# Performance work log

Hardware: AMD Instinct MI355X
Metric: run time of the kernel (lower is better)

## Reference

```python
import jax, jax.numpy as jnp
import numpy as np
from jax import lax

EPS = 1e-5
MIN_SAMPLES = 4
RESHAPE = 14        # edge-map downsample factor
KEEP_FRAC = 0.1     # 1 - quantile(0.9)
KERNEL_FRAC = 0.05  # eval-mode log_kernel

SOBEL_X = jnp.array([[-1., 0., 1.], [-2., 0., 2.], [-1., 0., 1.]], jnp.float32)
SOBEL_Y = jnp.array([[-1., -2., -1.], [0., 0., 0.], [1., 2., 1.]], jnp.float32)


def _dwconv3(x, k):
    C = x.shape[1]
    kern = jnp.broadcast_to(k, (C, 1, 3, 3)).astype(x.dtype)
    return lax.conv_general_dilated(x, kern, (1, 1), 'SAME',
        feature_group_count=C, dimension_numbers=('NCHW', 'OIHW', 'NCHW'))


def _erode3(m):
    k = jnp.ones((1, 1, 3, 3), m.dtype)
    s = lax.conv_general_dilated(m, k, (1, 1), 'SAME',
        dimension_numbers=('NCHW', 'OIHW', 'NCHW'))
    return (s >= 9.0).astype(m.dtype)


def _masked_mean(x, mask, axis=-1):
    m = mask.astype(x.dtype)
    return jnp.sum(x * m, axis=axis) / jnp.maximum(jnp.sum(m, axis=axis), 1.0)


def _ssi_norm(x, mask):
    # scale-shift-invariant normalization: masked median shift, masked MAD scale
    big = jnp.where(mask, x, jnp.inf)
    srt = jnp.sort(big, axis=-1)
    n = jnp.sum(mask, axis=-1)
    idx = jnp.maximum((n - 1) // 2, 0)
    med = jnp.take_along_axis(srt, idx[..., None], axis=-1)
    med = jnp.where(n[..., None] > 0, med, 0.0)
    scale = _masked_mean(jnp.abs(x - med), mask, axis=-1)[..., None]
    return (x - med) / jnp.maximum(scale, EPS)


def _get_edge(image, vmask):
    gx = _dwconv3(image, SOBEL_X) / 8.0
    gy = _dwconv3(image, SOBEL_Y) / 8.0
    gx = jnp.sqrt(jnp.mean(gx * gx, axis=1, keepdims=True))
    gy = jnp.sqrt(jnp.mean(gy * gy, axis=1, keepdims=True))
    edges = jnp.sqrt(gx * gx + gy * gy)
    H, W = edges.shape[-2:]
    bm = jnp.zeros((H, W), edges.dtype).at[3:H - 3, 3:W - 3].set(1.0)
    return edges * bm * vmask


def _resize_bilinear(x, oh, ow):
    # torch F.interpolate bilinear, align_corners=False, no antialias
    B, C, H, W = x.shape
    def coords(o, s):
        c = jnp.clip((jnp.arange(o) + 0.5) * (s / o) - 0.5, 0.0, s - 1.0)
        i0 = jnp.floor(c).astype(jnp.int32)
        return i0, jnp.minimum(i0 + 1, s - 1), c - i0
    y0, y1, wy = coords(oh, H)
    x0, x1, wx = coords(ow, W)
    wy = wy[:, None]; wx = wx[None, :]
    g = lambda yi, xi: x[:, :, yi[:, None], xi[None, :]]
    return (g(y0, x0) * (1 - wy) * (1 - wx) + g(y0, x1) * (1 - wy) * wx
          + g(y1, x0) * wy * (1 - wx) + g(y1, x1) * wy * wx)


def _sample_edges(edges):
    B, _, H, W = edges.shape
    oh, ow = H // RESHAPE, W // RESHAPE
    e = _resize_bilinear(edges, oh, ow).reshape(B, -1)
    k = max(int(KEEP_FRAC * oh * ow), 10)
    _, idx = lax.top_k(e, k)
    return jnp.stack([(idx // ow) * RESHAPE, (idx % ow) * RESHAPE], -1).astype(jnp.int32)


def _extract_patches(x, coords, kh, kw):
    # vectorized irregular patch gather: [B,C,H,W] + [B,P,2] -> [B,P*C,kh*kw]
    B, C, H, W = x.shape
    ph, pw = kh // 2, kw // 2
    xp = jnp.pad(x, ((0, 0), (0, 0), (ph, ph), (pw, pw)))
    dy = jnp.arange(-ph, ph + 1)
    dx = jnp.arange(-pw, pw + 1)
    def one(img, y, x_):
        return img[:, (y + dy)[:, None], (x_ + dx)[None, :]]
    patches = jax.vmap(jax.vmap(one, in_axes=(None, 0, 0)))(
        xp, coords[..., 0] + ph, coords[..., 1] + pw)  # [B,P,C,kh,kw]
    return patches.reshape(B, -1, kh * kw)


def _forward(inp, tgt, mask, image, vmask):
    mask = mask.astype(bool)
    inp = inp.astype(jnp.float32)
    tgt = tgt.astype(jnp.float32)
    B, _, H, W = inp.shape
    vm = _erode3(vmask.astype(jnp.float32))
    edges = _get_edge(image.astype(jnp.float32), vm)
    coords = _sample_edges(edges)
    ks = int(KERNEL_FRAC * min(H, W))
    ks += int(ks % 2 == 0)
    # local patch branch
    pin = _extract_patches(inp, coords, ks, ks)
    ptg = _extract_patches(tgt, coords, ks, ks)
    pmk = _extract_patches(mask.astype(jnp.float32), coords, ks, ks) > 0.5
    pin = _ssi_norm(pin, pmk)
    ptg = _ssi_norm(ptg, pmk)
    err = jnp.maximum(jnp.abs(pin - ptg), EPS)
    valid = jnp.sum(pmk, axis=-1) >= MIN_SAMPLES
    ep = jnp.sqrt(jnp.maximum(_masked_mean(err, pmk, -1), EPS))  # [B,P]
    e_patch = _masked_mean(ep, valid, -1)                         # [B]
    # global image branch
    gi = _ssi_norm(inp.reshape(B, 1, H * W), mask.reshape(B, 1, H * W))
    gt = _ssi_norm(tgt.reshape(B, 1, H * W), mask.reshape(B, 1, H * W))
    gerr = jnp.maximum(jnp.abs(gi - gt), EPS)
    e_glob = jnp.sqrt(jnp.maximum(_masked_mean(gerr, mask.reshape(B, 1, H * W), -1), EPS)).squeeze(-1)
    return 0.5 * (e_patch + e_glob)  # [B]


def setup_inputs() -> dict:
    key = jax.random.key(0)
    k1, k2, k3, k4 = jax.random.split(key, 4)
    B, H, W = 32, 480, 640
    return {
        'input': jax.random.uniform(k1, (B, 1, H, W), jnp.float32, 0.1, 10.0),
        'target': jax.random.uniform(k2, (B, 1, H, W), jnp.float32, 0.1, 10.0),
        'mask': jax.random.bernoulli(k3, 0.9, (B, 1, H, W)),
        'image': jax.random.normal(k4, (B, 3, H, W), jnp.float32),
        'validity_mask': jnp.ones((B, 1, H, W), bool),
    }


def reference(input, target, mask, image, validity_mask):
    return _forward(input, target, mask, image, validity_mask)
```

## Files before the change

### kernel.cpp

```cpp
#include <hip/hip_runtime.h>
#include <math.h>

#define BB 32
#define HH 480
#define WW 640
#define HWN (HH * WW)
#define OH 34
#define OW 45
#define OHW (OH * OW)
#define KTOP 153
#define KS 25
#define PHW 12
#define PATCH (KS * KS)
#define RESHAPE_I 14
#define EPSV 1e-5f

#define TSLICE 10
#define TSW (OHW / TSLICE)

#define NB12 4096
#define PSLICE 32
#define NSLICE 16
#define CAP 32768
#define LCAP 2048
#define CPAD 32

__device__ __forceinline__ unsigned int fkey(float f) {
  unsigned int u = __float_as_uint(f);
  return (u & 0x80000000u) ? ~u : (u | 0x80000000u);
}
__device__ __forceinline__ float fkey_inv(unsigned int k) {
  unsigned int u = (k & 0x80000000u) ? (k & 0x7FFFFFFFu) : ~k;
  return __uint_as_float(u);
}

__device__ __forceinline__ float breduce256(float v, float* red) {
  const int t = threadIdx.x;
  __syncthreads();
  red[t] = v;
  __syncthreads();
  for (int s2 = 128; s2 > 0; s2 >>= 1) {
    if (t < s2) red[t] += red[t + s2];
    __syncthreads();
  }
  float r = red[0];
  __syncthreads();
  return r;
}

__device__ __forceinline__ float2 breduce256x2(float a, float b, float* red) {
  const int t = threadIdx.x;
  __syncthreads();
  red[t] = a;
  red[256 + t] = b;
  __syncthreads();
  for (int s2 = 128; s2 > 0; s2 >>= 1) {
    if (t < s2) {
      red[t] += red[t + s2];
      red[256 + t] += red[256 + t + s2];
    }
    __syncthreads();
  }
  float2 r = make_float2(red[0], red[256]);
  __syncthreads();
  return r;
}

__device__ float edge_at(const float* __restrict__ image, const unsigned char* __restrict__ vmask,
                         int b, int y, int x) {
  if (y < 3 || y >= HH - 3 || x < 3 || x >= WW - 3) return 0.f;
  const unsigned char* vm = vmask + (size_t)b * HWN;
  #pragma unroll
  for (int dy = -1; dy <= 1; ++dy) {
    #pragma unroll
    for (int dx = -1; dx <= 1; ++dx) {
      if (!vm[(size_t)(y + dy) * WW + (x + dx)]) return 0.f;
    }
  }
  const float* img = image + (size_t)b * 3 * HWN;
  float sx2 = 0.f, sy2 = 0.f;
  #pragma unroll
  for (int c = 0; c < 3; ++c) {
    const float* p = img + (size_t)c * HWN + (size_t)y * WW + x;
    float a00 = p[-WW - 1], a01 = p[-WW], a02 = p[-WW + 1];
    float a10 = p[-1],                    a12 = p[1];
    float a20 = p[WW - 1],  a21 = p[WW],  a22 = p[WW + 1];
    float gx = (-a00 + a02 + -2.f * a10 + 2.f * a12 + -a20 + a22) / 8.f;
    float gy = (-a00 + -2.f * a01 + -a02 + a20 + 2.f * a21 + a22) / 8.f;
    sx2 += gx * gx;
    sy2 += gy * gy;
  }
  float gxm = sqrtf(sx2 / 3.f);
  float gym = sqrtf(sy2 / 3.f);
  return sqrtf(gxm * gxm + gym * gym);
}

__global__ __launch_bounds__(256) void edge_resize_kernel(const float* __restrict__ image,
                                                          const unsigned char* __restrict__ vmask,
                                                          float* __restrict__ re) {
  int gid = blockIdx.x * 256 + threadIdx.x;
  int corner = gid & 3;
  int cell = gid >> 2;
  int b = cell / OHW;
  int rem = cell % OHW;
  int oy = rem / OW, ox = rem % OW;

  const float ry = (float)((double)HH / (double)OH);
  const float rx = (float)((double)WW / (double)OW);
  float cy = fminf(fmaxf(((float)oy + 0.5f) * ry - 0.5f, 0.f), (float)(HH - 1));
  float cx = fminf(fmaxf(((float)ox + 0.5f) * rx - 0.5f, 0.f), (float)(WW - 1));
  int y0 = (int)floorf(cy);
  int x0 = (int)floorf(cx);
  int y1 = min(y0 + 1, HH - 1);
  int x1 = min(x0 + 1, WW - 1);
  float wy = cy - (float)y0;
  float wx = cx - (float)x0;

  int yy = (corner & 2) ? y1 : y0;
  int xx = (corner & 1) ? x1 : x0;
  float w = ((corner & 2) ? wy : 1.f - wy) * ((corner & 1) ? wx : 1.f - wx);
  float g = edge_at(image, vmask, b, yy, xx) * w;
  g += __shfl_xor(g, 1, 64);
  g += __shfl_xor(g, 2, 64);
  if (corner == 0) re[cell] = g;
}

__global__ __launch_bounds__(256) void topk_rank_kernel(const float* __restrict__ re,
                                                        int* __restrict__ rpart) {
  const int b = blockIdx.x / TSLICE;
  const int sl = blockIdx.x % TSLICE;
  const int t = threadIdx.x;
  __shared__ float e[OHW];
  for (int i = t; i < OHW; i += 256) e[i] = re[b * OHW + i];
  __syncthreads();

  float vi[6];
  int idx[6], cnt[6];
  #pragma unroll
  for (int q = 0; q < 6; ++q) {
    int i = t + q * 256;
    idx[q] = i;
    vi[q] = (i < OHW) ? e[i] : 0.f;
    cnt[q] = 0;
  }
  const int j0 = sl * TSW;
  for (int jj = 0; jj < TSW; ++jj) {
    int j = j0 + jj;
    float u = e[j];
    #pragma unroll
    for (int q = 0; q < 6; ++q) {
      cnt[q] += (u > vi[q]) || (u == vi[q] && j < idx[q]);
    }
  }
  int* rp = rpart + ((size_t)b * TSLICE + sl) * OHW;
  #pragma unroll
  for (int q = 0; q < 6; ++q) {
    if (idx[q] < OHW) rp[idx[q]] = cnt[q];
  }
}

__global__ __launch_bounds__(256) void topk_write_kernel(const int* __restrict__ rpart,
                                                         int* __restrict__ coords) {
  const int b = blockIdx.x;
  const int t = threadIdx.x;
  const int* rp = rpart + (size_t)b * TSLICE * OHW;
  for (int i = t; i < OHW; i += 256) {
    int rank = 0;
    #pragma unroll
    for (int sl = 0; sl < TSLICE; ++sl) rank += rp[sl * OHW + i];
    if (rank < KTOP) {
      coords[(b * KTOP + rank) * 2 + 0] = (i / OW) * RESHAPE_I;
      coords[(b * KTOP + rank) * 2 + 1] = (i % OW) * RESHAPE_I;
    }
  }
}

__global__ __launch_bounds__(64, 4) void patch_kernel(const float* __restrict__ inp,
                                                      const float* __restrict__ tgt,
                                                      const unsigned char* __restrict__ mask,
                                                      const int* __restrict__ coords,
                                                      float* __restrict__ ep, float* __restrict__ val) {
  const int bk = blockIdx.x;
  const int b = bk / KTOP;
  const int t = threadIdx.x;
  __shared__ unsigned int hist[512];
  __shared__ unsigned int sh_pref[2];
  __shared__ int sh_rank[2];

  const int cy = coords[bk * 2 + 0];
  const int cx = coords[bk * 2 + 1];

  float v_in[10], v_tg[10];
  unsigned int mbits = 0;
  #pragma unroll
  for (int q = 0; q < 10; ++q) {
    int i = t + q * 64;
    float vi = 0.f, vt = 0.f;
    if (i < PATCH) {
      int dy = i / KS - PHW, dx = i % KS - PHW;
      int y = cy + dy, x = cx + dx;
      if (y >= 0 && y < HH && x >= 0 && x < WW) {
        size_t off = (size_t)b * HWN + (size_t)y * WW + x;
        if (mask[off]) mbits |= (1u << q);
        vi = inp[off];
        vt = tgt[off];
      }
    }
    v_in[q] = vi; v_tg[q] = vt;
  }

  int pn = __popc(mbits);
  #pragma unroll
  for (int d = 32; d > 0; d >>= 1) pn += __shfl_xor(pn, d, 64);
  const int n = pn;
  const float nf = (float)n;
  const int r = (n > 0) ? ((n - 1) >> 1) : 0;

  if (t == 0) {
    sh_pref[0] = 0; sh_pref[1] = 0;
    sh_rank[0] = r; sh_rank[1] = r;
  }
  __syncthreads();

  #pragma unroll
  for (int p = 0; p < 4; ++p) {
    const int shift = 24 - 8 * p;
    #pragma unroll
    for (int j = 0; j < 8; ++j) hist[t + 64 * j] = 0;
    __syncthreads();
    const int r_in = sh_rank[0], r_tg = sh_rank[1];
    const unsigned int pref_in = sh_pref[0], pref_tg = sh_pref[1];
    #pragma unroll
    for (int q = 0; q < 10; ++q) {
      if (mbits & (1u << q)) {
        unsigned int k = fkey(v_in[q]);
        if (p == 0 || (k >> (shift + 8)) == pref_in)
          atomicAdd(&hist[(k >> shift) & 255u], 1u);
        unsigned int k2 = fkey(v_tg[q]);
        if (p == 0 || (k2 >> (shift + 8)) == pref_tg)
          atomicAdd(&hist[256 + ((k2 >> shift) & 255u)], 1u);
      }
    }
    __syncthreads();
    {
      unsigned int a0 = hist[t * 4 + 0], a1 = hist[t * 4 + 1];
      unsigned int a2 = hist[t * 4 + 2], a3 = hist[t * 4 + 3];
      unsigned int b0 = hist[256 + t * 4 + 0], b1 = hist[256 + t * 4 + 1];
      unsigned int b2 = hist[256 + t * 4 + 2], b3 = hist[256 + t * 4 + 3];
      unsigned int sa0 = a0, sa1 = sa0 + a1, sa2 = sa1 + a2, sa3 = sa2 + a3;
      unsigned int sb0 = b0, sb1 = sb0 + b1, sb2 = sb1 + b2, sb3 = sb2 + b3;
      unsigned int ta = sa3, tb = sb3;
      #pragma unroll
      for (int d = 1; d < 64; d <<= 1) {
        unsigned int ua = (unsigned int)__shfl_up((int)ta, d, 64);
        unsigned int ub = (unsigned int)__shfl_up((int)tb, d, 64);
        if (t >= d) { ta += ua; tb += ub; }
      }
      unsigned int exa = ta - sa3, exb = tb - sb3;
      unsigned int rra = (unsigned int)r_in, rrb = (unsigned int)r_tg;
      unsigned int pa[4] = {exa, exa + sa0, exa + sa1, exa + sa2};
      unsigned int ca[4] = {exa + sa0, exa + sa1, exa + sa2, exa + sa3};
      unsigned int pb[4] = {exb, exb + sb0, exb + sb1, exb + sb2};
      unsigned int cb[4] = {exb + sb0, exb + sb1, exb + sb2, exb + sb3};
      #pragma unroll
      for (int j = 0; j < 4; ++j) {
        if (rra >= pa[j] && rra < ca[j]) {
          sh_pref[0] = (pref_in << 8) | (unsigned int)(t * 4 + j);
          sh_rank[0] = (int)(rra - pa[j]);
        }
        if (rrb >= pb[j] && rrb < cb[j]) {
          sh_pref[1] = (pref_tg << 8) | (unsigned int)(t * 4 + j);
          sh_rank[1] = (int)(rrb - pb[j]);
        }
      }
    }
    __syncthreads();
  }

  const float med_i = (n > 0) ? fkey_inv(sh_pref[0]) : 0.f;
  const float med_t = (n > 0) ? fkey_inv(sh_pref[1]) : 0.f;

  float pi = 0.f, pt = 0.f;
  #pragma unroll
  for (int q = 0; q < 10; ++q) {
    if (mbits & (1u << q)) {
      pi += fabsf(v_in[q] - med_i);
      pt += fabsf(v_tg[q] - med_t);
    }
  }
  #pragma unroll
  for (int d = 32; d > 0; d >>= 1) {
    pi += __shfl_xor(pi, d, 64);
    pt += __shfl_xor(pt, d, 64);
  }
  const float si = fmaxf(pi / fmaxf(nf, 1.f), EPSV);
  const float st = fmaxf(pt / fmaxf(nf, 1.f), EPSV);

  float pe = 0.f;
  #pragma unroll
  for (int q = 0; q < 10; ++q) {
    if (mbits & (1u << q)) {
      float a = (v_in[q] - med_i) / si;
      float c = (v_tg[q] - med_t) / st;
      pe += fmaxf(fabsf(a - c), EPSV);
    }
  }
  #pragma unroll
  for (int d = 32; d > 0; d >>= 1) pe += __shfl_xor(pe, d, 64);

  if (t == 0) {
    ep[bk] = sqrtf(fmaxf(pe / fmaxf(nf, 1.f), EPSV));
    val[bk] = (n >= 4) ? 1.f : 0.f;
  }
}

__global__ __launch_bounds__(256) void preduce_kernel(const float* __restrict__ ep,
                                                      const float* __restrict__ val,
                                                      float* __restrict__ e_patch) {
  const int b = blockIdx.x;
  const int t = threadIdx.x;
  __shared__ float red[512];
  float se = 0.f, sv = 0.f;
  for (int i = t; i < KTOP; i += 256) {
    float v = val[b * KTOP + i];
    se += ep[b * KTOP + i] * v;
    sv += v;
  }
  float2 tt = breduce256x2(se, sv, red);
  if (t == 0) e_patch[b] = tt.x / fmaxf(tt.y, 1.f);
}

__global__ __launch_bounds__(256) void gpass12_kernel(const float* __restrict__ inp,
                                                      const float* __restrict__ tgt,
                                                      const unsigned char* __restrict__ mask,
                                                      unsigned int* __restrict__ ghist) {
  const int b = blockIdx.x / PSLICE;
  const int sl = blockIdx.x % PSLICE;
  const int t = threadIdx.x;
  __shared__ unsigned int hist[2 * NB12];
  for (int i = t; i < 2 * NB12; i += 256) hist[i] = 0;
  __syncthreads();
  const float4* xi4 = (const float4*)(inp + (size_t)b * HWN);
  const float4* xt4 = (const float4*)(tgt + (size_t)b * HWN);
  const unsigned int* m4 = (const unsigned int*)(mask + (size_t)b * HWN);
  const int per4 = (HWN / PSLICE) / 4;
  const int s0 = sl * per4;
  for (int i = s0 + t; i < s0 + per4; i += 256) {
    unsigned int mm = m4[i];
    if (!mm) continue;
    float4 a = xi4[i], c = xt4[i];
    if (mm & 0x000000FFu) { atomicAdd(&hist[fkey(a.x) >> 20], 1u); atomicAdd(&hist[NB12 + (fkey(c.x) >> 20)], 1u); }
    if (mm & 0x0000FF00u) { atomicAdd(&hist[fkey(a.y) >> 20], 1u); atomicAdd(&hist[NB12 + (fkey(c.y) >> 20)], 1u); }
    if (mm & 0x00FF0000u) { atomicAdd(&hist[fkey(a.z) >> 20], 1u); atomicAdd(&hist[NB12 + (fkey(c.z) >> 20)], 1u); }
    if (mm & 0xFF000000u) { atomicAdd(&hist[fkey(a.w) >> 20], 1u); atomicAdd(&hist[NB12 + (fkey(c.w) >> 20)], 1u); }
  }
  __syncthreads();
  for (int i = t; i < NB12; i += 256) {
    unsigned int h0 = hist[i], h1 = hist[NB12 + i];
    if (h0) atomicAdd(&ghist[(size_t)(b * 2 + 0) * NB12 + i], h0);
    if (h1) atomicAdd(&ghist[(size_t)(b * 2 + 1) * NB12 + i], h1);
  }
}

__global__ __launch_bounds__(256) void gsel12_kernel(const unsigned int* __restrict__ ghist,
                                                     int* __restrict__ sel) {
  const int bs = blockIdx.x;
  const int t = threadIdx.x;
  const unsigned int* gh = ghist + (size_t)bs * NB12;
  __shared__ unsigned int scan[256];
  unsigned int local[16];
  unsigned int s = 0;
  const int base = t * 16;
  #pragma unroll
  for (int j = 0; j < 16; ++j) {
    local[j] = gh[base + j];
    s += local[j];
  }
  scan[t] = s;
  __syncthreads();
  for (int d = 1; d < 256; d <<= 1) {
    unsigned int v = (t >= d) ? scan[t - d] : 0u;
    __syncthreads();
    scan[t] += v;
    __syncthreads();
  }
  const unsigned int incl = scan[t];
  const unsigned int ex = incl - s;
  const unsigned int n = scan[255];
  if (n == 0) {
    if (t == 0) {
      sel[bs * 4 + 0] = -1;
      sel[bs * 4 + 1] = 0;
      sel[bs * 4 + 2] = 0;
      sel[bs * 4 + 3] = 0;
    }
    return;
  }
  const unsigned int r = (n - 1) >> 1;
  if (r >= ex && r < incl) {
    unsigned int cum = ex;
    int bin = base;
    #pragma unroll
    for (int j = 0; j < 16; ++j) {
      unsigned int h = local[j];
      if (cum + h > r) { bin = base + j; break; }
      cum += h;
    }
    sel[bs * 4 + 0] = bin;
    sel[bs * 4 + 1] = (int)(r - cum);
    sel[bs * 4 + 2] = (int)n;
    sel[bs * 4 + 3] = (int)cum;
  }
}

__global__ __launch_bounds__(256) void gcollect_kernel(const float* __restrict__ inp,
                                                       const float* __restrict__ tgt,
                                                       const unsigned char* __restrict__ mask,
                                                       const int* __restrict__ sel,
                                                       float* __restrict__ cand,
                                                       unsigned int* __restrict__ ccount,
                                                       float* __restrict__ sbelow,
                                                       float* __restrict__ sabove) {
  const int bs = blockIdx.x / NSLICE;
  const int sl = blockIdx.x % NSLICE;
  const int b = bs >> 1, s = bs & 1;
  const float* x = (s == 0 ? inp : tgt) + (size_t)b * HWN;
  const unsigned char* m = mask + (size_t)b * HWN;
  const int prefix = sel[bs * 4 + 0];
  __shared__ float red[512];
  __shared__ float buf[LCAP];
  __shared__ unsigned int lcnt, gbase;
  const int t = threadIdx.x;
  if (t == 0) lcnt = 0;
  __syncthreads();
  float sb = 0.f, sa = 0.f;
  if (prefix >= 0) {
    float* cd = cand + (size_t)bs * CAP;
    const float4* x4 = (const float4*)x;
    const unsigned int* m4 = (const unsigned int*)m;
    const int per4 = (HWN / NSLICE) / 4;
    const int s0 = sl * per4;
    for (int i = s0 + t; i < s0 + per4; i += 256) {
      unsigned int mm = m4[i];
      if (!mm) continue;
      float4 a = x4[i];
      #define GCOL(av, bit) \
        if (mm & bit) { \
          float v = av; \
          int pf = (int)(fkey(v) >> 20); \
          if (pf < prefix) sb += v; \
          else if (pf > prefix) sa += v; \
          else { \
            unsigned int pos = atomicAdd(&lcnt, 1u); \
            if (pos < LCAP) buf[pos] = v; \
            else { \
              unsigned int g = atomicAdd(&ccount[bs * CPAD], 1u); \
              if (g < CAP) cd[g] = v; \
            } \
          } \
        }
      GCOL(a.x, 0x000000FFu)
      GCOL(a.y, 0x0000FF00u)
      GCOL(a.z, 0x00FF0000u)
      GCOL(a.w, 0xFF000000u)
      #undef GCOL
    }
  }
  __syncthreads();
  if (prefix >= 0) {
    unsigned int c = min(lcnt, (unsigned int)LCAP);
    if (t == 0 && c > 0) gbase = atomicAdd(&ccount[bs * CPAD], c);
    __syncthreads();
    if (c > 0) {
      float* cd = cand + (size_t)bs * CAP;
      unsigned int base = gbase;
      for (unsigned int i = t; i < c; i += 256) {
        unsigned int pos = base + i;
        if (pos < CAP) cd[pos] = buf[i];
      }
    }
  }
  float2 ts = breduce256x2(sb, sa, red);
  if (t == 0) {
    atomicAdd(&sbelow[bs], ts.x);
    atomicAdd(&sabove[bs], ts.y);
  }
}

__global__ __launch_bounds__(256) void gfinal_kernel(const float* __restrict__ cand,
                                                     const unsigned int* __restrict__ ccount,
                                                     const int* __restrict__ sel,
                                                     const float* __restrict__ sbelow,
                                                     const float* __restrict__ sabove,
                                                     float* __restrict__ gstats,
                                                     float* __restrict__ nvals) {
  const int bs = blockIdx.x;
  const int t = threadIdx.x;
  const int prefix = sel[bs * 4 + 0];
  const int r2 = sel[bs * 4 + 1];
  const int n = sel[bs * 4 + 2];
  const int nbelow = sel[bs * 4 + 3];
  __shared__ unsigned int hist[256];
  __shared__ float red[256];
  __shared__ int sh_bin, sh_r;
  __shared__ float sh_med;
  const float* cd = cand + (size_t)bs * CAP;
  int c = (int)min(ccount[bs * CPAD], (unsigned int)CAP);
  if (prefix < 0) {
    if (t == 0) {
      gstats[bs * 2 + 0] = 0.f;
      gstats[bs * 2 + 1] = 0.f;
      if ((bs & 1) == 0) nvals[bs >> 1] = 0.f;
    }
    return;
  }

  hist[t] = 0;
  __syncthreads();
  for (int i = t; i < c; i += 256)
    atomicAdd(&hist[(fkey(cd[i]) >> 12) & 255u], 1u);
  __syncthreads();
  if (t == 0) {
    unsigned int rr = (unsigned int)r2, cum = 0;
    int bin = 0;
    for (; bin < 256; ++bin) {
      unsigned int h = hist[bin];
      if (cum + h > rr) break;
      cum += h;
    }
    sh_bin = bin;
    sh_r = (int)(rr - cum);
  }
  __syncthreads();
  const int bin1 = sh_bin;
  const int r3 = sh_r;

  hist[t] = 0;
  __syncthreads();
  for (int i = t; i < c; i += 256) {
    unsigned int k = fkey(cd[i]);
    if (((k >> 12) & 255u) == (unsigned int)bin1)
      atomicAdd(&hist[(k >> 4) & 255u], 1u);
  }
  __syncthreads();
  if (t == 0) {
    unsigned int rr = (unsigned int)r3, cum = 0;
    int bin = 0;
    for (; bin < 256; ++bin) {
      unsigned int h = hist[bin];
      if (cum + h > rr) break;
      cum += h;
    }
    sh_bin = bin;
    sh_r = (int)(rr - cum);
  }
  __syncthreads();
  const int bin2 = sh_bin;
  const int r4 = sh_r;

  if (t < 16) hist[t] = 0;
  __syncthreads();
  {
    const unsigned int want = (((unsigned int)bin1 << 8) | (unsigned int)bin2);
    for (int i = t; i < c; i += 256) {
      unsigned int k = fkey(cd[i]);
      if (((k >> 4) & 0xFFFFu) == want)
        atomicAdd(&hist[k & 15u], 1u);
    }
  }
  __syncthreads();
  if (t == 0) {
    unsigned int rr = (unsigned int)r4, cum = 0;
    int bin = 0;
    for (; bin < 16; ++bin) {
      unsigned int h = hist[bin];
      if (cum + h > rr) break;
      cum += h;
    }
    unsigned int key = ((unsigned int)prefix << 20) |
                       ((unsigned int)bin1 << 12) |
                       ((unsigned int)bin2 << 4) | (unsigned int)bin;
    sh_med = fkey_inv(key);
  }
  __syncthreads();
  const float med = sh_med;

  float ps = 0.f;
  for (int i = t; i < c; i += 256) ps += fabsf(cd[i] - med);
  float scand = breduce256(ps, red);
  if (t == 0) {
    float nb = (float)nbelow;
    float na = (float)(n - nbelow - c);
    float num = (nb * med - sbelow[bs]) + (sabove[bs] - na * med) + scand;
    gstats[bs * 2 + 0] = med;
    gstats[bs * 2 + 1] = num / fmaxf((float)n, 1.f);
    if ((bs & 1) == 0) nvals[bs >> 1] = (float)n;
  }
}

__global__ __launch_bounds__(256) void gerr_kernel(const float* __restrict__ inp,
                                                   const float* __restrict__ tgt,
                                                   const unsigned char* __restrict__ mask,
                                                   const float* __restrict__ gstats,
                                                   float* __restrict__ gacc) {
  const int b = blockIdx.x / PSLICE;
  const int sl = blockIdx.x % PSLICE;
  __shared__ float red[256];
  const int t = threadIdx.x;
  const float med_i = gstats[(b * 2 + 0) * 2 + 0];
  const float sc_i = fmaxf(gstats[(b * 2 + 0) * 2 + 1], EPSV);
  const float med_t = gstats[(b * 2 + 1) * 2 + 0];
  const float sc_t = fmaxf(gstats[(b * 2 + 1) * 2 + 1], EPSV);
  const float ri = 1.f / sc_i, rt = 1.f / sc_t;
  const float4* xi4 = (const float4*)(inp + (size_t)b * HWN);
  const float4* xt4 = (const float4*)(tgt + (size_t)b * HWN);
  const unsigned int* m4 = (const unsigned int*)(mask + (size_t)b * HWN);
  const int per4 = (HWN / PSLICE) / 4;
  const int s0 = sl * per4;
  float part = 0.f;
  for (int i = s0 + t; i < s0 + per4; i += 256) {
    unsigned int mm = m4[i];
    if (!mm) continue;
    float4 a = xi4[i], c = xt4[i];
    if (mm & 0x000000FFu) part += fmaxf(fabsf((a.x - med_i) * ri - (c.x - med_t) * rt), EPSV);
    if (mm & 0x0000FF00u) part += fmaxf(fabsf((a.y - med_i) * ri - (c.y - med_t) * rt), EPSV);
    if (mm & 0x00FF0000u) part += fmaxf(fabsf((a.z - med_i) * ri - (c.z - med_t) * rt), EPSV);
    if (mm & 0xFF000000u) part += fmaxf(fabsf((a.w - med_i) * ri - (c.w - med_t) * rt), EPSV);
  }
  float tp = breduce256(part, red);
  if (t == 0) atomicAdd(&gacc[b], tp);
}

__global__ __launch_bounds__(64) void final_kernel(const float* __restrict__ gacc,
                                                   const float* __restrict__ nvals,
                                                   const float* __restrict__ e_patch,
                                                   float* __restrict__ out) {
  const int b = threadIdx.x;
  if (b < BB) {
    float n = nvals[b];
    float eg = sqrtf(fmaxf(gacc[b] / fmaxf(n, 1.f), EPSV));
    out[b] = 0.5f * (e_patch[b] + eg);
  }
}

extern "C" void kernel_launch(void* const* d_in, const int* in_sizes, int n_in,
                              void* d_out, int out_size, void* d_ws, size_t ws_size,
                              hipStream_t stream) {
  const float* inp = (const float*)d_in[0];
  const float* tgt = (const float*)d_in[1];
  const unsigned char* mask = (const unsigned char*)d_in[2];
  const float* image = (const float*)d_in[3];
  const unsigned char* vmask = (const unsigned char*)d_in[4];
  float* out = (float*)d_out;

  float* ws = (float*)d_ws;
  float* re = ws;
  int* coords = (int*)(ws + 48960);
  float* ep = ws + 48960 + 9792;
  float* val = ep + 4896;
  float* e_patch = val + 4896;
  float* gstats = e_patch + 32;
  float* nvals = gstats + 128;
  int* sel12 = (int*)(nvals + 32);
  float* cand = (float*)(sel12 + 256);
  unsigned int* ghist12 = (unsigned int*)(cand + (size_t)64 * CAP);
  unsigned int* ccount = ghist12 + (size_t)64 * NB12;
  float* sbelow = (float*)(ccount + 64 * CPAD);
  float* sabove = sbelow + 64;
  float* gacc = sabove + 64;
  size_t zero_bytes = ((size_t)64 * NB12 + 64 * CPAD + 64 + 64 + 32) * 4;
  hipMemsetAsync(ghist12, 0, zero_bytes, stream);

  int* rpart = (int*)cand;

  edge_resize_kernel<<<(BB * OHW * 4) / 256, 256, 0, stream>>>(image, vmask, re);
  topk_rank_kernel<<<BB * TSLICE, 256, 0, stream>>>(re, rpart);
  topk_write_kernel<<<BB, 256, 0, stream>>>(rpart, coords);
  patch_kernel<<<BB * KTOP, 64, 0, stream>>>(inp, tgt, mask, coords, ep, val);
  preduce_kernel<<<BB, 256, 0, stream>>>(ep, val, e_patch);
  gpass12_kernel<<<BB * PSLICE, 256, 0, stream>>>(inp, tgt, mask, ghist12);
  gsel12_kernel<<<BB * 2, 256, 0, stream>>>(ghist12, sel12);
  gcollect_kernel<<<BB * 2 * NSLICE, 256, 0, stream>>>(inp, tgt, mask, sel12, cand, ccount, sbelow, sabove);
  gfinal_kernel<<<BB * 2, 256, 0, stream>>>(cand, ccount, sel12, sbelow, sabove, gstats, nvals);
  gerr_kernel<<<BB * PSLICE, 256, 0, stream>>>(inp, tgt, mask, gstats, gacc);
  final_kernel<<<1, 64, 0, stream>>>(gacc, nvals, e_patch, out);
}
```

Baseline: 393.2 us.

## Merge independent kernels into shared launches and fold the final reduction into gerr

```diff
diff --git a/kernel.cpp b/kernel.cpp
--- a/kernel.cpp
+++ b/kernel.cpp
@@ -25,6 +25,10 @@
 #define LCAP 2048
 #define CPAD 32
 
+#define EDGE_BLKS ((BB * OHW * 4) / 256)
+#define RANK_BLKS (BB * TSLICE)
+#define COL_BLKS (BB * 2 * NSLICE)
+
 __device__ __forceinline__ unsigned int fkey(float f) {
   unsigned int u = __float_as_uint(f);
   return (u & 0x80000000u) ? ~u : (u | 0x80000000u);
@@ -93,6 +97,38 @@
   float gxm = sqrtf(sx2 / 3.f);
   float gym = sqrtf(sy2 / 3.f);
   return sqrtf(gxm * gxm + gym * gym);
+}
+
+__global__ __launch_bounds__(256) void gpass12_kernel(const float* __restrict__ inp,
+                                                      const float* __restrict__ tgt,
+                                                      const unsigned char* __restrict__ mask,
+                                                      unsigned int* __restrict__ ghist) {
+  const int b = blockIdx.x / PSLICE;
+  const int sl = blockIdx.x % PSLICE;
+  const int t = threadIdx.x;
+  __shared__ unsigned int hist[2 * NB12];
+  for (int i = t; i < 2 * NB12; i += 256) hist[i] = 0;
+  __syncthreads();
+  const float4* xi4 = (const float4*)(inp + (size_t)b * HWN);
+  const float4* xt4 = (const float4*)(tgt + (size_t)b * HWN);
+  const unsigned int* m4 = (const unsigned int*)(mask + (size_t)b * HWN);
+  const int per4 = (HWN / PSLICE) / 4;
+  const int s0 = sl * per4;
+  for (int i = s0 + t; i < s0 + per4; i += 256) {
+    unsigned int mm = m4[i];
+    if (!mm) continue;
+    float4 a = xi4[i], c = xt4[i];
+    if (mm & 0x000000FFu) { atomicAdd(&hist[fkey(a.x) >> 20], 1u); atomicAdd(&hist[NB12 + (fkey(c.x) >> 20)], 1u); }
+    if (mm & 0x0000FF00u) { atomicAdd(&hist[fkey(a.y) >> 20], 1u); atomicAdd(&hist[NB12 + (fkey(c.y) >> 20)], 1u); }
+    if (mm & 0x00FF0000u) { atomicAdd(&hist[fkey(a.z) >> 20], 1u); atomicAdd(&hist[NB12 + (fkey(c.z) >> 20)], 1u); }
+    if (mm & 0xFF000000u) { atomicAdd(&hist[fkey(a.w) >> 20], 1u); atomicAdd(&hist[NB12 + (fkey(c.w) >> 20)], 1u); }
+  }
+  __syncthreads();
+  for (int i = t; i < NB12; i += 256) {
+    unsigned int h0 = hist[i], h1 = hist[NB12 + i];
+    if (h0) atomicAdd(&ghist[(size_t)(b * 2 + 0) * NB12 + i], h0);
+    if (h1) atomicAdd(&ghist[(size_t)(b * 2 + 1) * NB12 + i], h1);
+  }
 }
 
 __global__ __launch_bounds__(256) void edge_resize_kernel(const float* __restrict__ image,
@@ -125,52 +161,177 @@
   if (corner == 0) re[cell] = g;
 }
 
-__global__ __launch_bounds__(256) void topk_rank_kernel(const float* __restrict__ re,
-                                                        int* __restrict__ rpart) {
-  const int b = blockIdx.x / TSLICE;
-  const int sl = blockIdx.x % TSLICE;
-  const int t = threadIdx.x;
+__global__ __launch_bounds__(256) void k_rank_sel(const float* __restrict__ re,
+                                                  const unsigned int* __restrict__ ghist,
+                                                  int* __restrict__ rpart,
+                                                  int* __restrict__ sel) {
   __shared__ float e[OHW];
-  for (int i = t; i < OHW; i += 256) e[i] = re[b * OHW + i];
-  __syncthreads();
-
-  float vi[6];
-  int idx[6], cnt[6];
-  #pragma unroll
-  for (int q = 0; q < 6; ++q) {
-    int i = t + q * 256;
-    idx[q] = i;
-    vi[q] = (i < OHW) ? e[i] : 0.f;
-    cnt[q] = 0;
-  }
-  const int j0 = sl * TSW;
-  for (int jj = 0; jj < TSW; ++jj) {
-    int j = j0 + jj;
-    float u = e[j];
+  __shared__ unsigned int scan[256];
+  const int t = threadIdx.x;
+  if (blockIdx.x < RANK_BLKS) {
+    const int b = blockIdx.x / TSLICE;
+    const int sl = blockIdx.x % TSLICE;
+    for (int i = t; i < OHW; i += 256) e[i] = re[b * OHW + i];
+    __syncthreads();
+
+    float vi[6];
+    int idx[6], cnt[6];
     #pragma unroll
     for (int q = 0; q < 6; ++q) {
-      cnt[q] += (u > vi[q]) || (u == vi[q] && j < idx[q]);
-    }
-  }
-  int* rp = rpart + ((size_t)b * TSLICE + sl) * OHW;
-  #pragma unroll
-  for (int q = 0; q < 6; ++q) {
-    if (idx[q] < OHW) rp[idx[q]] = cnt[q];
-  }
-}
-
-__global__ __launch_bounds__(256) void topk_write_kernel(const int* __restrict__ rpart,
-                                                         int* __restrict__ coords) {
-  const int b = blockIdx.x;
-  const int t = threadIdx.x;
-  const int* rp = rpart + (size_t)b * TSLICE * OHW;
-  for (int i = t; i < OHW; i += 256) {
-    int rank = 0;
+      int i = t + q * 256;
+      idx[q] = i;
+      vi[q] = (i < OHW) ? e[i] : 0.f;
+      cnt[q] = 0;
+    }
+    const int j0 = sl * TSW;
+    for (int jj = 0; jj < TSW; ++jj) {
+      int j = j0 + jj;
+      float u = e[j];
+      #pragma unroll
+      for (int q = 0; q < 6; ++q) {
+        cnt[q] += (u > vi[q]) || (u == vi[q] && j < idx[q]);
+      }
+    }
+    int* rp = rpart + ((size_t)b * TSLICE + sl) * OHW;
     #pragma unroll
-    for (int sl = 0; sl < TSLICE; ++sl) rank += rp[sl * OHW + i];
-    if (rank < KTOP) {
-      coords[(b * KTOP + rank) * 2 + 0] = (i / OW) * RESHAPE_I;
-      coords[(b * KTOP + rank) * 2 + 1] = (i % OW) * RESHAPE_I;
+    for (int q = 0; q < 6; ++q) {
+      if (idx[q] < OHW) rp[idx[q]] = cnt[q];
+    }
+  } else {
+    const int bs = blockIdx.x - RANK_BLKS;
+    const unsigned int* gh = ghist + (size_t)bs * NB12;
+    unsigned int local[16];
+    unsigned int s = 0;
+    const int base = t * 16;
+    #pragma unroll
+    for (int j = 0; j < 16; ++j) {
+      local[j] = gh[base + j];
+      s += local[j];
+    }
+    scan[t] = s;
+    __syncthreads();
+    for (int d = 1; d < 256; d <<= 1) {
+      unsigned int v = (t >= d) ? scan[t - d] : 0u;
+      __syncthreads();
+      scan[t] += v;
+      __syncthreads();
+    }
+    const unsigned int incl = scan[t];
+    const unsigned int ex = incl - s;
+    const unsigned int n = scan[255];
+    if (n == 0) {
+      if (t == 0) {
+        sel[bs * 4 + 0] = -1;
+        sel[bs * 4 + 1] = 0;
+        sel[bs * 4 + 2] = 0;
+        sel[bs * 4 + 3] = 0;
+      }
+      return;
+    }
+    const unsigned int r = (n - 1) >> 1;
+    if (r >= ex && r < incl) {
+      unsigned int cum = ex;
+      int bin = base;
+      #pragma unroll
+      for (int j = 0; j < 16; ++j) {
+        unsigned int h = local[j];
+        if (cum + h > r) { bin = base + j; break; }
+        cum += h;
+      }
+      sel[bs * 4 + 0] = bin;
+      sel[bs * 4 + 1] = (int)(r - cum);
+      sel[bs * 4 + 2] = (int)n;
+      sel[bs * 4 + 3] = (int)cum;
+    }
+  }
+}
+
+__global__ __launch_bounds__(256) void k_write_collect(const float* __restrict__ inp,
+                                                       const float* __restrict__ tgt,
+                                                       const unsigned char* __restrict__ mask,
+                                                       const int* __restrict__ sel,
+                                                       const int* __restrict__ rpart,
+                                                       float* __restrict__ cand,
+                                                       unsigned int* __restrict__ ccount,
+                                                       float* __restrict__ sbelow,
+                                                       float* __restrict__ sabove,
+                                                       int* __restrict__ coords) {
+  __shared__ float red[512];
+  __shared__ float buf[LCAP];
+  __shared__ unsigned int lcnt, gbase;
+  const int t = threadIdx.x;
+  if (blockIdx.x < COL_BLKS) {
+    const int bs = blockIdx.x / NSLICE;
+    const int sl = blockIdx.x % NSLICE;
+    const int b = bs >> 1, s = bs & 1;
+    const float* x = (s == 0 ? inp : tgt) + (size_t)b * HWN;
+    const unsigned char* m = mask + (size_t)b * HWN;
+    const int prefix = sel[bs * 4 + 0];
+    if (t == 0) lcnt = 0;
+    __syncthreads();
+    float sb = 0.f, sa = 0.f;
+    if (prefix >= 0) {
+      float* cd = cand + (size_t)bs * CAP;
+      const float4* x4 = (const float4*)x;
+      const unsigned int* m4 = (const unsigned int*)m;
+      const int per4 = (HWN / NSLICE) / 4;
+      const int s0 = sl * per4;
+      for (int i = s0 + t; i < s0 + per4; i += 256) {
+        unsigned int mm = m4[i];
+        if (!mm) continue;
+        float4 a = x4[i];
+        #define GCOL(av, bit) \
+          if (mm & bit) { \
+            float v = av; \
+            int pf = (int)(fkey(v) >> 20); \
+            if (pf < prefix) sb += v; \
+            else if (pf > prefix) sa += v; \
+            else { \
+              unsigned int pos = atomicAdd(&lcnt, 1u); \
+              if (pos < LCAP) buf[pos] = v; \
+              else { \
+                unsigned int g = atomicAdd(&ccount[bs * CPAD], 1u); \
+                if (g < CAP) cd[g] = v; \
+              } \
+            } \
+          }
+        GCOL(a.x, 0x000000FFu)
+        GCOL(a.y, 0x0000FF00u)
+        GCOL(a.z, 0x00FF0000u)
+        GCOL(a.w, 0xFF000000u)
+        #undef GCOL
+      }
+    }
+    __syncthreads();
+    if (prefix >= 0) {
+      unsigned int c = min(lcnt, (unsigned int)LCAP);
+      if (t == 0 && c > 0) gbase = atomicAdd(&ccount[bs * CPAD], c);
+      __syncthreads();
+      if (c > 0) {
+        float* cd = cand + (size_t)bs * CAP;
+        unsigned int base = gbase;
+        for (unsigned int i = t; i < c; i += 256) {
+          unsigned int pos = base + i;
+          if (pos < CAP) cd[pos] = buf[i];
+        }
+      }
+    }
+    float2 ts = breduce256x2(sb, sa, red);
+    if (t == 0) {
+      atomicAdd(&sbelow[bs], ts.x);
+      atomicAdd(&sabove[bs], ts.y);
+    }
+  } else {
+    const int b = blockIdx.x - COL_BLKS;
+    const int* rp = rpart + (size_t)b * TSLICE * OHW;
+    for (int i = t; i < OHW; i += 256) {
+      int rank = 0;
+      #pragma unroll
+      for (int sl = 0; sl < TSLICE; ++sl) rank += rp[sl * OHW + i];
+      if (rank < KTOP) {
+        coords[(b * KTOP + rank) * 2 + 0] = (i / OW) * RESHAPE_I;
+        coords[(b * KTOP + rank) * 2 + 1] = (i % OW) * RESHAPE_I;
+      }
     }
   }
 }
@@ -314,295 +475,141 @@
   }
 }
 
-__global__ __launch_bounds__(256) void preduce_kernel(const float* __restrict__ ep,
-                                                      const float* __restrict__ val,
-                                                      float* __restrict__ e_patch) {
-  const int b = blockIdx.x;
-  const int t = threadIdx.x;
+__global__ __launch_bounds__(256) void k_gfinal_preduce(const float* __restrict__ cand,
+                                                        const unsigned int* __restrict__ ccount,
+                                                        const int* __restrict__ sel,
+                                                        const float* __restrict__ sbelow,
+                                                        const float* __restrict__ sabove,
+                                                        const float* __restrict__ ep,
+                                                        const float* __restrict__ val,
+                                                        float* __restrict__ gstats,
+                                                        float* __restrict__ nvals,
+                                                        float* __restrict__ e_patch) {
+  __shared__ unsigned int hist[256];
   __shared__ float red[512];
-  float se = 0.f, sv = 0.f;
-  for (int i = t; i < KTOP; i += 256) {
-    float v = val[b * KTOP + i];
-    se += ep[b * KTOP + i] * v;
-    sv += v;
-  }
-  float2 tt = breduce256x2(se, sv, red);
-  if (t == 0) e_patch[b] = tt.x / fmaxf(tt.y, 1.f);
-}
-
-__global__ __launch_bounds__(256) void gpass12_kernel(const float* __restrict__ inp,
-                                                      const float* __restrict__ tgt,
-                                                      const unsigned char* __restrict__ mask,
-                                                      unsigned int* __restrict__ ghist) {
-  const int b = blockIdx.x / PSLICE;
-  const int sl = blockIdx.x % PSLICE;
-  const int t = threadIdx.x;
-  __shared__ unsigned int hist[2 * NB12];
-  for (int i = t; i < 2 * NB12; i += 256) hist[i] = 0;
-  __syncthreads();
-  const float4* xi4 = (const float4*)(inp + (size_t)b * HWN);
-  const float4* xt4 = (const float4*)(tgt + (size_t)b * HWN);
-  const unsigned int* m4 = (const unsigned int*)(mask + (size_t)b * HWN);
-  const int per4 = (HWN / PSLICE) / 4;
-  const int s0 = sl * per4;
-  for (int i = s0 + t; i < s0 + per4; i += 256) {
-    unsigned int mm = m4[i];
-    if (!mm) continue;
-    float4 a = xi4[i], c = xt4[i];
-    if (mm & 0x000000FFu) { atomicAdd(&hist[fkey(a.x) >> 20], 1u); atomicAdd(&hist[NB12 + (fkey(c.x) >> 20)], 1u); }
-    if (mm & 0x0000FF00u) { atomicAdd(&hist[fkey(a.y) >> 20], 1u); atomicAdd(&hist[NB12 + (fkey(c.y) >> 20)], 1u); }
-    if (mm & 0x00FF0000u) { atomicAdd(&hist[fkey(a.z) >> 20], 1u); atomicAdd(&hist[NB12 + (fkey(c.z) >> 20)], 1u); }
-    if (mm & 0xFF000000u) { atomicAdd(&hist[fkey(a.w) >> 20], 1u); atomicAdd(&hist[NB12 + (fkey(c.w) >> 20)], 1u); }
-  }
-  __syncthreads();
-  for (int i = t; i < NB12; i += 256) {
-    unsigned int h0 = hist[i], h1 = hist[NB12 + i];
-    if (h0) atomicAdd(&ghist[(size_t)(b * 2 + 0) * NB12 + i], h0);
-    if (h1) atomicAdd(&ghist[(size_t)(b * 2 + 1) * NB12 + i], h1);
-  }
-}
-
-__global__ __launch_bounds__(256) void gsel12_kernel(const unsigned int* __restrict__ ghist,
-                                                     int* __restrict__ sel) {
-  const int bs = blockIdx.x;
-  const int t = threadIdx.x;
-  const unsigned int* gh = ghist + (size_t)bs * NB12;
-  __shared__ unsigned int scan[256];
-  unsigned int local[16];
-  unsigned int s = 0;
-  const int base = t * 16;
-  #pragma unroll
-  for (int j = 0; j < 16; ++j) {
-    local[j] = gh[base + j];
-    s += local[j];
-  }
-  scan[t] = s;
-  __syncthreads();
-  for (int d = 1; d < 256; d <<= 1) {
-    unsigned int v = (t >= d) ? scan[t - d] : 0u;
-    __syncthreads();
-    scan[t] += v;
-    __syncthreads();
-  }
-  const unsigned int incl = scan[t];
-  const unsigned int ex = incl - s;
-  const unsigned int n = scan[255];
-  if (n == 0) {
-    if (t == 0) {
-      sel[bs * 4 + 0] = -1;
-      sel[bs * 4 + 1] = 0;
-      sel[bs * 4 + 2] = 0;
-      sel[bs * 4 + 3] = 0;
-    }
-    return;
-  }
-  const unsigned int r = (n - 1) >> 1;
-  if (r >= ex && r < incl) {
-    unsigned int cum = ex;
-    int bin = base;
-    #pragma unroll
-    for (int j = 0; j < 16; ++j) {
-      unsigned int h = local[j];
-      if (cum + h > r) { bin = base + j; break; }
-      cum += h;
-    }
-    sel[bs * 4 + 0] = bin;
-    sel[bs * 4 + 1] = (int)(r - cum);
-    sel[bs * 4 + 2] = (int)n;
-    sel[bs * 4 + 3] = (int)cum;
-  }
-}
-
-__global__ __launch_bounds__(256) void gcollect_kernel(const float* __restrict__ inp,
-                                                       const float* __restrict__ tgt,
-                                                       const unsigned char* __restrict__ mask,
-                                                       const int* __restrict__ sel,
-                                                       float* __restrict__ cand,
-                                                       unsigned int* __restrict__ ccount,
-                                                       float* __restrict__ sbelow,
-                                                       float* __restrict__ sabove) {
-  const int bs = blockIdx.x / NSLICE;
-  const int sl = blockIdx.x % NSLICE;
-  const int b = bs >> 1, s = bs & 1;
-  const float* x = (s == 0 ? inp : tgt) + (size_t)b * HWN;
-  const unsigned char* m = mask + (size_t)b * HWN;
-  const int prefix = sel[bs * 4 + 0];
-  __shared__ float red[512];
-  __shared__ float buf[LCAP];
-  __shared__ unsigned int lcnt, gbase;
-  const int t = threadIdx.x;
-  if (t == 0) lcnt = 0;
-  __syncthreads();
-  float sb = 0.f, sa = 0.f;
-  if (prefix >= 0) {
-    float* cd = cand + (size_t)bs * CAP;
-    const float4* x4 = (const float4*)x;
-    const unsigned int* m4 = (const unsigned int*)m;
-    const int per4 = (HWN / NSLICE) / 4;
-    const int s0 = sl * per4;
-    for (int i = s0 + t; i < s0 + per4; i += 256) {
-      unsigned int mm = m4[i];
-      if (!mm) continue;
-      float4 a = x4[i];
-      #define GCOL(av, bit) \
-        if (mm & bit) { \
-          float v = av; \
-          int pf = (int)(fkey(v) >> 20); \
-          if (pf < prefix) sb += v; \
-          else if (pf > prefix) sa += v; \
-          else { \
-            unsigned int pos = atomicAdd(&lcnt, 1u); \
-            if (pos < LCAP) buf[pos] = v; \
-            else { \
-              unsigned int g = atomicAdd(&ccount[bs * CPAD], 1u); \
-              if (g < CAP) cd[g] = v; \
-            } \
-          } \
-        }
-      GCOL(a.x, 0x000000FFu)
-      GCOL(a.y, 0x0000FF00u)
-      GCOL(a.z, 0x00FF0000u)
-      GCOL(a.w, 0xFF000000u)
-      #undef GCOL
-    }
-  }
-  __syncthreads();
-  if (prefix >= 0) {
-    unsigned int c = min(lcnt, (unsigned int)LCAP);
-    if (t == 0 && c > 0) gbase = atomicAdd(&ccount[bs * CPAD], c);
-    __syncthreads();
-    if (c > 0) {
-      float* cd = cand + (size_t)bs * CAP;
-      unsigned int base = gbase;
-      for (unsigned int i = t; i < c; i += 256) {
-        unsigned int pos = base + i;
-        if (pos < CAP) cd[pos] = buf[i];
-      }
-    }
-  }
-  float2 ts = breduce256x2(sb, sa, red);
-  if (t == 0) {
-    atomicAdd(&sbelow[bs], ts.x);
-    atomicAdd(&sabove[bs], ts.y);
-  }
-}
-
-__global__ __launch_bounds__(256) void gfinal_kernel(const float* __restrict__ cand,
-                                                     const unsigned int* __restrict__ ccount,
-                                                     const int* __restrict__ sel,
-                                                     const float* __restrict__ sbelow,
-                                                     const float* __restrict__ sabove,
-                                                     float* __restrict__ gstats,
-                                                     float* __restrict__ nvals) {
-  const int bs = blockIdx.x;
-  const int t = threadIdx.x;
-  const int prefix = sel[bs * 4 + 0];
-  const int r2 = sel[bs * 4 + 1];
-  const int n = sel[bs * 4 + 2];
-  const int nbelow = sel[bs * 4 + 3];
-  __shared__ unsigned int hist[256];
-  __shared__ float red[256];
   __shared__ int sh_bin, sh_r;
   __shared__ float sh_med;
-  const float* cd = cand + (size_t)bs * CAP;
-  int c = (int)min(ccount[bs * CPAD], (unsigned int)CAP);
-  if (prefix < 0) {
+  const int t = threadIdx.x;
+  if (blockIdx.x < 64) {
+    const int bs = blockIdx.x;
+    const int prefix = sel[bs * 4 + 0];
+    const int r2 = sel[bs * 4 + 1];
+    const int n = sel[bs * 4 + 2];
+    const int nbelow = sel[bs * 4 + 3];
+    const float* cd = cand + (size_t)bs * CAP;
+    int c = (int)min(ccount[bs * CPAD], (unsigned int)CAP);
+    if (prefix < 0) {
+      if (t == 0) {
+        gstats[bs * 2 + 0] = 0.f;
+        gstats[bs * 2 + 1] = 0.f;
+        if ((bs & 1) == 0) nvals[bs >> 1] = 0.f;
+      }
+      return;
+    }
+
+    hist[t] = 0;
+    __syncthreads();
+    for (int i = t; i < c; i += 256)
+      atomicAdd(&hist[(fkey(cd[i]) >> 12) & 255u], 1u);
+    __syncthreads();
     if (t == 0) {
-      gstats[bs * 2 + 0] = 0.f;
-      gstats[bs * 2 + 1] = 0.f;
-      if ((bs & 1) == 0) nvals[bs >> 1] = 0.f;
-    }
-    return;
-  }
-
-  hist[t] = 0;
-  __syncthreads();
-  for (int i = t; i < c; i += 256)
-    atomicAdd(&hist[(fkey(cd[i]) >> 12) & 255u], 1u);
-  __syncthreads();
-  if (t == 0) {
-    unsigned int rr = (unsigned int)r2, cum = 0;
-    int bin = 0;
-    for (; bin < 256; ++bin) {
-      unsigned int h = hist[bin];
-      if (cum + h > rr) break;
-      cum += h;
-    }
-    sh_bin = bin;
-    sh_r = (int)(rr - cum);
-  }
-  __syncthreads();
-  const int bin1 = sh_bin;
-  const int r3 = sh_r;
-
-  hist[t] = 0;
-  __syncthreads();
-  for (int i = t; i < c; i += 256) {
-    unsigned int k = fkey(cd[i]);
-    if (((k >> 12) & 255u) == (unsigned int)bin1)
-      atomicAdd(&hist[(k >> 4) & 255u], 1u);
-  }
-  __syncthreads();
-  if (t == 0) {
-    unsigned int rr = (unsigned int)r3, cum = 0;
-    int bin = 0;
-    for (; bin < 256; ++bin) {
-      unsigned int h = hist[bin];
-      if (cum + h > rr) break;
-      cum += h;
-    }
-    sh_bin = bin;
-    sh_r = (int)(rr - cum);
-  }
-  __syncthreads();
-  const int bin2 = sh_bin;
-  const int r4 = sh_r;
-
-  if (t < 16) hist[t] = 0;
-  __syncthreads();
-  {
-    const unsigned int want = (((unsigned int)bin1 << 8) | (unsigned int)bin2);
+      unsigned int rr = (unsigned int)r2, cum = 0;
+      int bin = 0;
+      for (; bin < 256; ++bin) {
+        unsigned int h = hist[bin];
+        if (cum + h > rr) break;
+        cum += h;
+      }
+      sh_bin = bin;
+      sh_r = (int)(rr - cum);
+    }
+    __syncthreads();
+    const int bin1 = sh_bin;
+    const int r3 = sh_r;
+
+    hist[t] = 0;
+    __syncthreads();
     for (int i = t; i < c; i += 256) {
       unsigned int k = fkey(cd[i]);
-      if (((k >> 4) & 0xFFFFu) == want)
-        atomicAdd(&hist[k & 15u], 1u);
-    }
-  }
-  __syncthreads();
-  if (t == 0) {
-    unsigned int rr = (unsigned int)r4, cum = 0;
-    int bin = 0;
-    for (; bin < 16; ++bin) {
-      unsigned int h = hist[bin];
-      if (cum + h > rr) break;
-      cum += h;
-    }
-    unsigned int key = ((unsigned int)prefix << 20) |
-                       ((unsigned int)bin1 << 12) |
-                       ((unsigned int)bin2 << 4) | (unsigned int)bin;
-    sh_med = fkey_inv(key);
-  }
-  __syncthreads();
-  const float med = sh_med;
-
-  float ps = 0.f;
-  for (int i = t; i < c; i += 256) ps += fabsf(cd[i] - med);
-  float scand = breduce256(ps, red);
-  if (t == 0) {
-    float nb = (float)nbelow;
-    float na = (float)(n - nbelow - c);
-    float num = (nb * med - sbelow[bs]) + (sabove[bs] - na * med) + scand;
-    gstats[bs * 2 + 0] = med;
-    gstats[bs * 2 + 1] = num / fmaxf((float)n, 1.f);
-    if ((bs & 1) == 0) nvals[bs >> 1] = (float)n;
-  }
-}
-
-__global__ __launch_bounds__(256) void gerr_kernel(const float* __restrict__ inp,
-                                                   const float* __restrict__ tgt,
-                                                   const unsigned char* __restrict__ mask,
-                                                   const float* __restrict__ gstats,
-                                                   float* __restrict__ gacc) {
+      if (((k >> 12) & 255u) == (unsigned int)bin1)
+        atomicAdd(&hist[(k >> 4) & 255u], 1u);
+    }
+    __syncthreads();
+    if (t == 0) {
+      unsigned int rr = (unsigned int)r3, cum = 0;
+      int bin = 0;
+      for (; bin < 256; ++bin) {
+        unsigned int h = hist[bin];
+        if (cum + h > rr) break;
+        cum += h;
+      }
+      sh_bin = bin;
+      sh_r = (int)(rr - cum);
+    }
+    __syncthreads();
+    const int bin2 = sh_bin;
+    const int r4 = sh_r;
+
+    if (t < 16) hist[t] = 0;
+    __syncthreads();
+    {
+      const unsigned int want = (((unsigned int)bin1 << 8) | (unsigned int)bin2);
+      for (int i = t; i < c; i += 256) {
+        unsigned int k = fkey(cd[i]);
+        if (((k >> 4) & 0xFFFFu) == want)
+          atomicAdd(&hist[k & 15u], 1u);
+      }
+    }
+    __syncthreads();
+    if (t == 0) {
+      unsigned int rr = (unsigned int)r4, cum = 0;
+      int bin = 0;
+      for (; bin < 16; ++bin) {
+        unsigned int h = hist[bin];
+        if (cum + h > rr) break;
+        cum += h;
+      }
+      unsigned int key = ((unsigned int)prefix << 20) |
+                         ((unsigned int)bin1 << 12) |
+                         ((unsigned int)bin2 << 4) | (unsigned int)bin;
+      sh_med = fkey_inv(key);
+    }
+    __syncthreads();
+    const float med = sh_med;
+
+    float ps = 0.f;
+    for (int i = t; i < c; i += 256) ps += fabsf(cd[i] - med);
+    float scand = breduce256(ps, red);
+    if (t == 0) {
+      float nb = (float)nbelow;
+      float na = (float)(n - nbelow - c);
+      float num = (nb * med - sbelow[bs]) + (sabove[bs] - na * med) + scand;
+      gstats[bs * 2 + 0] = med;
+      gstats[bs * 2 + 1] = num / fmaxf((float)n, 1.f);
+      if ((bs & 1) == 0) nvals[bs >> 1] = (float)n;
+    }
+  } else {
+    const int b = blockIdx.x - 64;
+    float se = 0.f, sv = 0.f;
+    for (int i = t; i < KTOP; i += 256) {
+      float v = val[b * KTOP + i];
+      se += ep[b * KTOP + i] * v;
+      sv += v;
+    }
+    float2 tt = breduce256x2(se, sv, red);
+    if (t == 0) e_patch[b] = tt.x / fmaxf(tt.y, 1.f);
+  }
+}
+
+__global__ __launch_bounds__(256) void k_gerr_final(const float* __restrict__ inp,
+                                                    const float* __restrict__ tgt,
+                                                    const unsigned char* __restrict__ mask,
+                                                    const float* __restrict__ gstats,
+                                                    const float* __restrict__ nvals,
+                                                    const float* __restrict__ e_patch,
+                                                    float* __restrict__ gacc,
+                                                    unsigned int* __restrict__ gdone,
+                                                    float* __restrict__ out) {
   const int b = blockIdx.x / PSLICE;
   const int sl = blockIdx.x % PSLICE;
   __shared__ float red[256];
@@ -628,18 +635,17 @@
     if (mm & 0xFF000000u) part += fmaxf(fabsf((a.w - med_i) * ri - (c.w - med_t) * rt), EPSV);
   }
   float tp = breduce256(part, red);
-  if (t == 0) atomicAdd(&gacc[b], tp);
-}
-
-__global__ __launch_bounds__(64) void final_kernel(const float* __restrict__ gacc,
-                                                   const float* __restrict__ nvals,
-                                                   const float* __restrict__ e_patch,
-                                                   float* __restrict__ out) {
-  const int b = threadIdx.x;
-  if (b < BB) {
-    float n = nvals[b];
-    float eg = sqrtf(fmaxf(gacc[b] / fmaxf(n, 1.f), EPSV));
-    out[b] = 0.5f * (e_patch[b] + eg);
+  if (t == 0) {
+    atomicAdd(&gacc[b], tp);
+    __threadfence();
+    unsigned int prev = atomicAdd(&gdone[b], 1u);
+    if (prev == PSLICE - 1) {
+      __threadfence();
+      float g = atomicAdd(&gacc[b], 0.0f);
+      float n = nvals[b];
+      float eg = sqrtf(fmaxf(g / fmaxf(n, 1.f), EPSV));
+      out[b] = 0.5f * (e_patch[b] + eg);
+    }
   }
 }
 
@@ -656,32 +662,31 @@
   float* ws = (float*)d_ws;
   float* re = ws;
   int* coords = (int*)(ws + 48960);
-  float* ep = ws + 48960 + 9792;
+  float* ep = (float*)(coords + 9792);
   float* val = ep + 4896;
   float* e_patch = val + 4896;
   float* gstats = e_patch + 32;
   float* nvals = gstats + 128;
   int* sel12 = (int*)(nvals + 32);
-  float* cand = (float*)(sel12 + 256);
+  int* rpart = sel12 + 256;
+  float* cand = (float*)(rpart + 489600);
   unsigned int* ghist12 = (unsigned int*)(cand + (size_t)64 * CAP);
   unsigned int* ccount = ghist12 + (size_t)64 * NB12;
   float* sbelow = (float*)(ccount + 64 * CPAD);
   float* sabove = sbelow + 64;
   float* gacc = sabove + 64;
-  size_t zero_bytes = ((size_t)64 * NB12 + 64 * CPAD + 64 + 64 + 32) * 4;
+  unsigned int* gdone = (unsigned int*)(gacc + 32);
+  size_t zero_bytes = ((size_t)64 * NB12 + 64 * CPAD + 64 + 64 + 32 + 32) * 4;
   hipMemsetAsync(ghist12, 0, zero_bytes, stream);
 
-  int* rpart = (int*)cand;
-
-  edge_resize_kernel<<<(BB * OHW * 4) / 256, 256, 0, stream>>>(image, vmask, re);
-  topk_rank_kernel<<<BB * TSLICE, 256, 0, stream>>>(re, rpart);
-  topk_write_kernel<<<BB, 256, 0, stream>>>(rpart, coords);
+  gpass12_kernel<<<BB * PSLICE, 256, 0, stream>>>(inp, tgt, mask, ghist12);
+  edge_resize_kernel<<<EDGE_BLKS, 256, 0, stream>>>(image, vmask, re);
+  k_rank_sel<<<RANK_BLKS + 64, 256, 0, stream>>>(re, ghist12, rpart, sel12);
+  k_write_collect<<<COL_BLKS + BB, 256, 0, stream>>>(inp, tgt, mask, sel12, rpart, cand, ccount,
+                                                     sbelow, sabove, coords);
   patch_kernel<<<BB * KTOP, 64, 0, stream>>>(inp, tgt, mask, coords, ep, val);
-  preduce_kernel<<<BB, 256, 0, stream>>>(ep, val, e_patch);
-  gpass12_kernel<<<BB * PSLICE, 256, 0, stream>>>(inp, tgt, mask, ghist12);
-  gsel12_kernel<<<BB * 2, 256, 0, stream>>>(ghist12, sel12);
-  gcollect_kernel<<<BB * 2 * NSLICE, 256, 0, stream>>>(inp, tgt, mask, sel12, cand, ccount, sbelow, sabove);
-  gfinal_kernel<<<BB * 2, 256, 0, stream>>>(cand, ccount, sel12, sbelow, sabove, gstats, nvals);
-  gerr_kernel<<<BB * PSLICE, 256, 0, stream>>>(inp, tgt, mask, gstats, gacc);
-  final_kernel<<<1, 64, 0, stream>>>(gacc, nvals, e_patch, out);
-}
+  k_gfinal_preduce<<<64 + BB, 256, 0, stream>>>(cand, ccount, sel12, sbelow, sabove,
+                                                ep, val, gstats, nvals, e_patch);
+  k_gerr_final<<<BB * PSLICE, 256, 0, stream>>>(inp, tgt, mask, gstats, nvals, e_patch,
+                                                gacc, gdone, out);
+}
```

Result: no change. 394.2 us, median of 2 (+0.2%).
